# Optimization experiments

Hardware: AMD Instinct MI355X
Metric: run time of the kernel (lower is better)

The kernel has to match this reference:

```python
import jax, jax.numpy as jnp
import numpy as np

B, C, H, W = 4, 256, 64, 64
C8 = C // 8


def setup_inputs() -> dict:
    key = jax.random.key(0)
    ks = jax.random.split(key, 8)
    x = jax.random.normal(ks[0], (B, C, H, W), dtype=jnp.float32)
    # 1x1 conv weights act as per-pixel linear maps: [out_ch, in_ch]
    Wq = jax.random.normal(ks[1], (C8, C), dtype=jnp.float32) * 0.05
    bq = jax.random.normal(ks[2], (C8,), dtype=jnp.float32) * 0.01
    Wk = jax.random.normal(ks[3], (C8, C), dtype=jnp.float32) * 0.05
    bk = jax.random.normal(ks[4], (C8,), dtype=jnp.float32) * 0.01
    Wv = jax.random.normal(ks[5], (C, C), dtype=jnp.float32) * 0.05
    bv = jax.random.normal(ks[6], (C,), dtype=jnp.float32) * 0.01
    # torch inits gamma to 0 (identity); use nonzero so output exercises the attention path
    gamma = jnp.array(0.5, dtype=jnp.float32)
    return {"x": x, "Wq": Wq, "bq": bq, "Wk": Wk, "bk": bk, "Wv": Wv, "bv": bv, "gamma": gamma}


def reference(x, Wq, bq, Wk, bk, Wv, bv, gamma):
    b, c, h, w = x.shape
    n = h * w
    xf = x.reshape(b, c, n)                                   # [B,C,N]
    q = jnp.einsum('oc,bcn->bno', Wq, xf) + bq                # [B,N,C8] (proj_query permuted)
    k = jnp.einsum('oc,bcn->bon', Wk, xf) + bk[:, None]       # [B,C8,N]
    energy = jnp.einsum('bnc,bcm->bnm', q, k)                 # [B,N_q,N_k]
    # NOTE: torch Softmax(dim=1) -> normalize over the QUERY axis (axis=1)
    attention = jax.nn.softmax(energy, axis=1)
    v = jnp.einsum('oc,bcn->bon', Wv, xf) + bv[:, None]       # [B,C,N]
    out = jnp.einsum('bcn,bnm->bcm', v, attention).reshape(b, c, h, w)
    return gamma * out + x
```

## Files before the change

### kernel.cpp

```cpp
#include <hip/hip_runtime.h>
#include <hip/hip_bf16.h>

#define BN 4
#define CC 256
#define C8 32
#define NN 4096
#define PROJ_ROWS 320

typedef __attribute__((ext_vector_type(8))) short short8;
typedef __attribute__((ext_vector_type(4))) float f32x4;

__device__ __forceinline__ unsigned short f2bf(float f) {
    unsigned u = __builtin_bit_cast(unsigned, f);
    unsigned r = (u + 0x7fffu + ((u >> 16) & 1u)) >> 16;
    return (unsigned short)r;
}

__global__ __launch_bounds__(256) void proj_kernel(
    const float* __restrict__ x,
    const float* __restrict__ Wq, const float* __restrict__ bq,
    const float* __restrict__ Wk, const float* __restrict__ bk,
    const float* __restrict__ Wv, const float* __restrict__ bv,
    unsigned short* __restrict__ proj, unsigned short* __restrict__ qT)
{
    int bid = blockIdx.x;
    int b = bid >> 6, nt = bid & 63;
    int n0 = nt * 64;
    int tid = threadIdx.x;
    int w = tid >> 6, l = tid & 63, l15 = l & 15, lq = l >> 4;

    __shared__ alignas(16) unsigned short Xt[64][264];

    int c_l = tid >> 3;
    int nb  = (tid & 7) * 8;

#pragma unroll
    for (int kc = 0; kc < 8; kc++) {
        const float* xp = x + ((size_t)(b * CC + kc * 32 + c_l)) * NN + n0 + nb;
        float4 x0 = *(const float4*)xp;
        float4 x1 = *(const float4*)(xp + 4);
        float t[8] = {x0.x, x0.y, x0.z, x0.w, x1.x, x1.y, x1.z, x1.w};
#pragma unroll
        for (int e = 0; e < 8; e++) Xt[nb + e][kc * 32 + c_l] = f2bf(t[e]);
    }
    __syncthreads();

    f32x4 acc[5][4];
#pragma unroll
    for (int gi = 0; gi < 5; gi++)
#pragma unroll
        for (int mi = 0; mi < 4; mi++) acc[gi][mi] = (f32x4){0.f, 0.f, 0.f, 0.f};

    for (int kc = 0; kc < 8; kc++) {
        float4 wf[5][2];
#pragma unroll
        for (int gi = 0; gi < 5; gi++) {
            int og = (w * 5 + gi) * 16 + l15;
            const float* wrow = (og < 32) ? (Wq + (size_t)og * CC)
                              : (og < 64) ? (Wk + (size_t)(og - 32) * CC)
                                          : (Wv + (size_t)(og - 64) * CC);
            const float* wp = wrow + kc * 32 + lq * 8;
            wf[gi][0] = *(const float4*)wp;
            wf[gi][1] = *(const float4*)(wp + 4);
        }
#pragma unroll
        for (int gi = 0; gi < 5; gi++) {
            unsigned short a8[8] __attribute__((aligned(16)));
            float tw[8] = {wf[gi][0].x, wf[gi][0].y, wf[gi][0].z, wf[gi][0].w,
                           wf[gi][1].x, wf[gi][1].y, wf[gi][1].z, wf[gi][1].w};
#pragma unroll
            for (int e = 0; e < 8; e++) a8[e] = f2bf(tw[e]);
            short8 af = *(const short8*)a8;
#pragma unroll
            for (int mi = 0; mi < 4; mi++) {
                short8 bf = *(const short8*)&Xt[mi * 16 + l15][kc * 32 + lq * 8];
                acc[gi][mi] = __builtin_amdgcn_mfma_f32_16x16x32_bf16(af, bf, acc[gi][mi], 0, 0, 0);
            }
        }
    }

#pragma unroll
    for (int gi = 0; gi < 5; gi++) {
#pragma unroll
        for (int r = 0; r < 4; r++) {
            int og = (w * 5 + gi) * 16 + lq * 4 + r;
            float bias = (og < 32) ? bq[og] : (og < 64) ? bk[og - 32] : bv[og - 64];
#pragma unroll
            for (int mi = 0; mi < 4; mi++) {
                int n = n0 + mi * 16 + l15;
                unsigned short v16 = f2bf(acc[gi][mi][r] + bias);
                if (og < 32) {
                    qT[((size_t)b * NN + n) * C8 + og] = v16;
                } else {
                    proj[((size_t)b * PROJ_ROWS + og) * NN + n] = v16;
                }
            }
        }
    }
}

template<int NSPLIT, bool FINAL>
__global__ __launch_bounds__(256, 4) void attn_kernel(
    const unsigned short* __restrict__ proj,
    const unsigned short* __restrict__ qT,
    const float* __restrict__ x,
    const float* __restrict__ gamma_p,
    float* __restrict__ out,
    float* __restrict__ Opart,
    float* __restrict__ Lpart)
{
    constexpr int ITERS = 64 / NSPLIT;
    int bid = blockIdx.x;
    int h   = bid >> 8;
    int low = bid & 255;
    int xcd = low & 7;
    int b = xcd >> 1;
    int mtile = ((low >> 3) << 1) | (xcd & 1);
    int m0 = mtile * 64;
    int nbase = h * (ITERS * 64);

    int tid = threadIdx.x;
    int w = tid >> 6, l = tid & 63, l15 = l & 15, lq = l >> 4;

    __shared__ alignas(16) unsigned short ps[2][64][72];
    __shared__ float red[4][64];
    __shared__ float Ltot[64];

    const unsigned short* kbase = proj + ((size_t)b * PROJ_ROWS + C8) * NN;
    const unsigned short* vbase = proj + ((size_t)b * PROJ_ROWS + 64) * NN;
    const unsigned short* qbase = qT + (size_t)b * NN * C8;

    short8 kfrag[4];
#pragma unroll
    for (int mi = 0; mi < 4; mi++) {
        int col = m0 + mi * 16 + l15;
        unsigned short t8[8] __attribute__((aligned(16)));
#pragma unroll
        for (int j = 0; j < 8; j++)
            t8[j] = kbase[(size_t)(lq * 8 + j) * NN + col];
        kfrag[mi] = *(const short8*)t8;
    }

    f32x4 O[4][4];
#pragma unroll
    for (int ci = 0; ci < 4; ci++)
#pragma unroll
        for (int mi = 0; mi < 4; mi++) O[ci][mi] = (f32x4){0.f, 0.f, 0.f, 0.f};
    float runS[4] = {0.f, 0.f, 0.f, 0.f};

    {
        short8 qfrag = *(const short8*)(qbase + (size_t)(nbase + 16 * w + l15) * C8 + lq * 8);
#pragma unroll
        for (int mi = 0; mi < 4; mi++) {
            f32x4 S = __builtin_amdgcn_mfma_f32_16x16x32_bf16(
                qfrag, kfrag[mi], (f32x4){0.f, 0.f, 0.f, 0.f}, 0, 0, 0);
            float p0 = __expf(S[0]);
            float p1 = __expf(S[1]);
            float p2 = __expf(S[2]);
            float p3 = __expf(S[3]);
            runS[mi] += (p0 + p1) + (p2 + p3);
            unsigned pk0 = (unsigned)f2bf(p0) | ((unsigned)f2bf(p1) << 16);
            unsigned pk1 = (unsigned)f2bf(p2) | ((unsigned)f2bf(p3) << 16);
            *(uint2*)&ps[0][mi * 16 + l15][16 * w + lq * 4] = make_uint2(pk0, pk1);
        }
    }

    for (int it = 0; it < ITERS; it++) {
        int n0c = nbase + it * 64;
        __syncthreads();

        const unsigned short* psrc = &ps[it & 1][0][0];
#pragma unroll
        for (int kh = 0; kh < 2; kh++) {
            short8 av[4];
#pragma unroll
            for (int ci = 0; ci < 4; ci++)
                av[ci] = *(const short8*)(vbase
                         + (size_t)(64 * w + ci * 16 + l15) * NN + n0c + kh * 32 + lq * 8);
            short8 bfr[4];
#pragma unroll
            for (int mi = 0; mi < 4; mi++)
                bfr[mi] = *(const short8*)(psrc + (mi * 16 + l15) * 72 + kh * 32 + lq * 8);
#pragma unroll
            for (int ci = 0; ci < 4; ci++)
#pragma unroll
                for (int mi = 0; mi < 4; mi++)
                    O[ci][mi] = __builtin_amdgcn_mfma_f32_16x16x32_bf16(
                        av[ci], bfr[mi], O[ci][mi], 0, 0, 0);
        }

        if (it + 1 < ITERS) {
            short8 qfrag = *(const short8*)(qbase
                           + (size_t)(n0c + 64 + 16 * w + l15) * C8 + lq * 8);
            unsigned short* pdst = &ps[(it + 1) & 1][0][0];
#pragma unroll
            for (int mi = 0; mi < 4; mi++) {
                f32x4 S = __builtin_amdgcn_mfma_f32_16x16x32_bf16(
                    qfrag, kfrag[mi], (f32x4){0.f, 0.f, 0.f, 0.f}, 0, 0, 0);
                float p0 = __expf(S[0]);
                float p1 = __expf(S[1]);
                float p2 = __expf(S[2]);
                float p3 = __expf(S[3]);
                runS[mi] += (p0 + p1) + (p2 + p3);
                unsigned pk0 = (unsigned)f2bf(p0) | ((unsigned)f2bf(p1) << 16);
                unsigned pk1 = (unsigned)f2bf(p2) | ((unsigned)f2bf(p3) << 16);
                *(uint2*)(pdst + (mi * 16 + l15) * 72 + 16 * w + lq * 4) = make_uint2(pk0, pk1);
            }
        }
    }

#pragma unroll
    for (int mi = 0; mi < 4; mi++) {
        float s = runS[mi];
        s += __shfl_xor(s, 16);
        s += __shfl_xor(s, 32);
        red[w][mi * 16 + l15] = s;
    }
    __syncthreads();
    if (tid < 64) Ltot[tid] = red[0][tid] + red[1][tid] + red[2][tid] + red[3][tid];
    __syncthreads();

    if constexpr (FINAL) {
        float gamma = gamma_p[0];
        float iv[4];
#pragma unroll
        for (int mi = 0; mi < 4; mi++) iv[mi] = 1.0f / Ltot[mi * 16 + l15];
#pragma unroll
        for (int ci = 0; ci < 4; ci++) {
#pragma unroll
            for (int mi = 0; mi < 4; mi++) {
                int m = m0 + mi * 16 + l15;
#pragma unroll
                for (int r = 0; r < 4; r++) {
                    int c = 64 * w + ci * 16 + lq * 4 + r;
                    size_t idx = ((size_t)b * CC + c) * NN + m;
                    out[idx] = gamma * (O[ci][mi][r] * iv[mi]) + x[idx];
                }
            }
        }
    } else {
        size_t p = ((size_t)h * BN + b) * 64 + mtile;
        if (tid < 64) Lpart[p * 64 + tid] = Ltot[tid];
        float* Ob = Opart + p * (size_t)(CC * 64);
#pragma unroll
        for (int ci = 0; ci < 4; ci++) {
#pragma unroll
            for (int mi = 0; mi < 4; mi++) {
#pragma unroll
                for (int r = 0; r < 4; r++) {
                    int c = 64 * w + ci * 16 + lq * 4 + r;
                    Ob[c * 64 + mi * 16 + l15] = O[ci][mi][r];
                }
            }
        }
    }
}

template<int NSPLIT>
__global__ __launch_bounds__(256) void combine_kernel(
    const float* __restrict__ Opart, const float* __restrict__ Lpart,
    const float* __restrict__ x, const float* __restrict__ gamma_p,
    float* __restrict__ out)
{
    int bid = blockIdx.x;
    int cq = bid & 3;
    int mt = (bid >> 2) & 63;
    int b  = bid >> 8;
    int tid = threadIdx.x;
    int m4 = tid & 15, c16 = tid >> 4;
    float gamma = gamma_p[0];

    f32x4 Ls = (f32x4){0.f, 0.f, 0.f, 0.f};
#pragma unroll
    for (int h = 0; h < NSPLIT; h++) {
        size_t p = ((size_t)h * BN + b) * 64 + mt;
        Ls += *(const f32x4*)(Lpart + p * 64 + m4 * 4);
    }
    f32x4 inv;
#pragma unroll
    for (int j = 0; j < 4; j++) inv[j] = 1.0f / Ls[j];

#pragma unroll
    for (int cp = 0; cp < 4; cp++) {
        int c = cq * 64 + cp * 16 + c16;
        f32x4 acc = (f32x4){0.f, 0.f, 0.f, 0.f};
#pragma unroll
        for (int h = 0; h < NSPLIT; h++) {
            size_t p = ((size_t)h * BN + b) * 64 + mt;
            acc += *(const f32x4*)(Opart + p * (size_t)(CC * 64) + c * 64 + m4 * 4);
        }
        size_t idx = ((size_t)b * CC + c) * NN + mt * 64 + m4 * 4;
        f32x4 xv = *(const f32x4*)(x + idx);
        f32x4 o;
#pragma unroll
        for (int j = 0; j < 4; j++) o[j] = gamma * (acc[j] * inv[j]) + xv[j];
        *(f32x4*)(out + idx) = o;
    }
}

extern "C" void kernel_launch(void* const* d_in, const int* in_sizes, int n_in,
                              void* d_out, int out_size, void* d_ws, size_t ws_size,
                              hipStream_t stream) {
    const float* x     = (const float*)d_in[0];
    const float* Wq    = (const float*)d_in[1];
    const float* bq    = (const float*)d_in[2];
    const float* Wk    = (const float*)d_in[3];
    const float* bk    = (const float*)d_in[4];
    const float* Wv    = (const float*)d_in[5];
    const float* bv    = (const float*)d_in[6];
    const float* gamma = (const float*)d_in[7];
    float* out = (float*)d_out;
    (void)in_sizes; (void)n_in; (void)out_size;

    unsigned short* proj = (unsigned short*)d_ws;
    unsigned short* qT   = proj + (size_t)BN * PROJ_ROWS * NN;
    const size_t baseB = ((size_t)BN * PROJ_ROWS * NN + (size_t)BN * NN * C8) * 2;

    auto needB = [&](int ns) {
        size_t LpB = (size_t)ns * BN * 64 * 64 * 4;
        size_t OpB = (size_t)ns * BN * 64 * CC * 64 * 4;
        return baseB + LpB + OpB;
    };

    proj_kernel<<<256, 256, 0, stream>>>(x, Wq, bq, Wk, bk, Wv, bv, proj, qT);

    if (ws_size >= needB(4)) {
        float* Lpart = (float*)((char*)d_ws + baseB);
        float* Opart = Lpart + (size_t)4 * BN * 64 * 64;
        attn_kernel<4, false><<<1024, 256, 0, stream>>>(proj, qT, x, gamma, out, Opart, Lpart);
        combine_kernel<4><<<1024, 256, 0, stream>>>(Opart, Lpart, x, gamma, out);
    } else if (ws_size >= needB(2)) {
        float* Lpart = (float*)((char*)d_ws + baseB);
        float* Opart = Lpart + (size_t)2 * BN * 64 * 64;
        attn_kernel<2, false><<<512, 256, 0, stream>>>(proj, qT, x, gamma, out, Opart, Lpart);
        combine_kernel<2><<<1024, 256, 0, stream>>>(Opart, Lpart, x, gamma, out);
    } else {
        attn_kernel<1, true><<<256, 256, 0, stream>>>(proj, qT, x, gamma, out, nullptr, nullptr);
    }
}
```

Baseline: 181.7 us.

## Restructure attention into single-wave blocks with register-resident P and exp2 softmax

The attention kernel becomes one wavefront per block. Each block owns 128 channels and 64 key columns and walks the query axis 16 rows at a time. The P tile stays in registers and feeds a 16x16x16 MFMA directly, which removes the LDS round-trip and the per-iteration __syncthreads. V and Q fragments for the next step are prefetched into registers. The projection folds log2(e) into K so the kernel can use exp2f, and it now uses smaller 32-column tiles with twice as many blocks. The trade-offs are that every channel-half block recomputes the QK^T energies and the exponentials, and the kernel carries high register pressure from 32 accumulators plus the prefetch buffers.

```diff
diff --git a/kernel.cpp b/kernel.cpp
--- a/kernel.cpp
+++ b/kernel.cpp
@@ -6,14 +6,26 @@
 #define C8 32
 #define NN 4096
 #define PROJ_ROWS 320
+#define LOG2E 1.4426950408889634f
 
 typedef __attribute__((ext_vector_type(8))) short short8;
+typedef __attribute__((ext_vector_type(4))) short short4v;
 typedef __attribute__((ext_vector_type(4))) float f32x4;
+typedef __attribute__((ext_vector_type(2))) unsigned int uint2v;
 
 __device__ __forceinline__ unsigned short f2bf(float f) {
     unsigned u = __builtin_bit_cast(unsigned, f);
     unsigned r = (u + 0x7fffu + ((u >> 16) & 1u)) >> 16;
     return (unsigned short)r;
+}
+
+__device__ __forceinline__ f32x4 mfma16_bf16(short4v a, short4v b, f32x4 c) {
+#if __has_builtin(__builtin_amdgcn_mfma_f32_16x16x16bf16_1k)
+    return __builtin_amdgcn_mfma_f32_16x16x16bf16_1k(a, b, c, 0, 0, 0);
+#else
+    asm("v_mfma_f32_16x16x16_bf16 %0, %1, %2, %0" : "+v"(c) : "v"(a), "v"(b));
+    return c;
+#endif
 }
 
 __global__ __launch_bounds__(256) void proj_kernel(
@@ -24,32 +36,32 @@
     unsigned short* __restrict__ proj, unsigned short* __restrict__ qT)
 {
     int bid = blockIdx.x;
-    int b = bid >> 6, nt = bid & 63;
-    int n0 = nt * 64;
+    int b = bid >> 7, nt = bid & 127;
+    int n0 = nt * 32;
     int tid = threadIdx.x;
     int w = tid >> 6, l = tid & 63, l15 = l & 15, lq = l >> 4;
 
-    __shared__ alignas(16) unsigned short Xt[64][264];
+    __shared__ alignas(16) unsigned short Xt[32][264];
 
     int c_l = tid >> 3;
-    int nb  = (tid & 7) * 8;
+    int nb  = (tid & 7) * 4;
 
 #pragma unroll
     for (int kc = 0; kc < 8; kc++) {
         const float* xp = x + ((size_t)(b * CC + kc * 32 + c_l)) * NN + n0 + nb;
         float4 x0 = *(const float4*)xp;
-        float4 x1 = *(const float4*)(xp + 4);
-        float t[8] = {x0.x, x0.y, x0.z, x0.w, x1.x, x1.y, x1.z, x1.w};
-#pragma unroll
-        for (int e = 0; e < 8; e++) Xt[nb + e][kc * 32 + c_l] = f2bf(t[e]);
+        Xt[nb + 0][kc * 32 + c_l] = f2bf(x0.x);
+        Xt[nb + 1][kc * 32 + c_l] = f2bf(x0.y);
+        Xt[nb + 2][kc * 32 + c_l] = f2bf(x0.z);
+        Xt[nb + 3][kc * 32 + c_l] = f2bf(x0.w);
     }
     __syncthreads();
 
-    f32x4 acc[5][4];
+    f32x4 acc[5][2];
 #pragma unroll
     for (int gi = 0; gi < 5; gi++)
 #pragma unroll
-        for (int mi = 0; mi < 4; mi++) acc[gi][mi] = (f32x4){0.f, 0.f, 0.f, 0.f};
+        for (int mi = 0; mi < 2; mi++) acc[gi][mi] = (f32x4){0.f, 0.f, 0.f, 0.f};
 
     for (int kc = 0; kc < 8; kc++) {
         float4 wf[5][2];
@@ -72,7 +84,7 @@
             for (int e = 0; e < 8; e++) a8[e] = f2bf(tw[e]);
             short8 af = *(const short8*)a8;
 #pragma unroll
-            for (int mi = 0; mi < 4; mi++) {
+            for (int mi = 0; mi < 2; mi++) {
                 short8 bf = *(const short8*)&Xt[mi * 16 + l15][kc * 32 + lq * 8];
                 acc[gi][mi] = __builtin_amdgcn_mfma_f32_16x16x32_bf16(af, bf, acc[gi][mi], 0, 0, 0);
             }
@@ -85,10 +97,13 @@
         for (int r = 0; r < 4; r++) {
             int og = (w * 5 + gi) * 16 + lq * 4 + r;
             float bias = (og < 32) ? bq[og] : (og < 64) ? bk[og - 32] : bv[og - 64];
-#pragma unroll
-            for (int mi = 0; mi < 4; mi++) {
+            bool is_k = (og >= 32) && (og < 64);
+#pragma unroll
+            for (int mi = 0; mi < 2; mi++) {
                 int n = n0 + mi * 16 + l15;
-                unsigned short v16 = f2bf(acc[gi][mi][r] + bias);
+                float v = acc[gi][mi][r] + bias;
+                if (is_k) v *= LOG2E;
+                unsigned short v16 = f2bf(v);
                 if (og < 32) {
                     qT[((size_t)b * NN + n) * C8 + og] = v16;
                 } else {
@@ -100,7 +115,7 @@
 }
 
 template<int NSPLIT, bool FINAL>
-__global__ __launch_bounds__(256, 4) void attn_kernel(
+__global__ __launch_bounds__(64, 2) void attn_kernel(
     const unsigned short* __restrict__ proj,
     const unsigned short* __restrict__ qT,
     const float* __restrict__ x,
@@ -109,22 +124,20 @@
     float* __restrict__ Opart,
     float* __restrict__ Lpart)
 {
-    constexpr int ITERS = 64 / NSPLIT;
+    constexpr int ITERS = NN / NSPLIT / 16;
     int bid = blockIdx.x;
-    int h   = bid >> 8;
-    int low = bid & 255;
-    int xcd = low & 7;
-    int b = xcd >> 1;
-    int mtile = ((low >> 3) << 1) | (xcd & 1);
-    int m0 = mtile * 64;
-    int nbase = h * (ITERS * 64);
-
-    int tid = threadIdx.x;
-    int w = tid >> 6, l = tid & 63, l15 = l & 15, lq = l >> 4;
-
-    __shared__ alignas(16) unsigned short ps[2][64][72];
-    __shared__ float red[4][64];
-    __shared__ float Ltot[64];
+    int low = bid & 7;
+    int b = low >> 1, mhalf = low & 1;
+    int rest = bid >> 3;
+    int h  = rest % NSPLIT;
+    int ch = (rest / NSPLIT) & 1;
+    int mt = ((rest / (NSPLIT * 2)) << 1) | mhalf;
+    int m0 = mt * 64;
+    int c0 = ch * 128;
+    int nbase = h * (NN / NSPLIT);
+
+    int l = threadIdx.x;
+    int l15 = l & 15, lq = l >> 4;
 
     const unsigned short* kbase = proj + ((size_t)b * PROJ_ROWS + C8) * NN;
     const unsigned short* vbase = proj + ((size_t)b * PROJ_ROWS + 64) * NN;
@@ -141,71 +154,64 @@
         kfrag[mi] = *(const short8*)t8;
     }
 
-    f32x4 O[4][4];
-#pragma unroll
-    for (int ci = 0; ci < 4; ci++)
+    f32x4 O[8][4];
+#pragma unroll
+    for (int ci = 0; ci < 8; ci++)
 #pragma unroll
         for (int mi = 0; mi < 4; mi++) O[ci][mi] = (f32x4){0.f, 0.f, 0.f, 0.f};
     float runS[4] = {0.f, 0.f, 0.f, 0.f};
 
-    {
-        short8 qfrag = *(const short8*)(qbase + (size_t)(nbase + 16 * w + l15) * C8 + lq * 8);
+    uint2v av[8];
+#pragma unroll
+    for (int ci = 0; ci < 8; ci++)
+        av[ci] = *(const uint2v*)(vbase + (size_t)(c0 + ci * 16 + l15) * NN + nbase + lq * 4);
+    short8 qfrag = *(const short8*)(qbase + (size_t)(nbase + l15) * C8 + lq * 8);
+
+    for (int it = 0; it < ITERS; it++) {
+        int n0c = nbase + it * 16;
+
+        uint2v avn[8];
+        short8 qn;
+        if (it + 1 < ITERS) {
+            int nn = n0c + 16;
+#pragma unroll
+            for (int ci = 0; ci < 8; ci++)
+                avn[ci] = *(const uint2v*)(vbase + (size_t)(c0 + ci * 16 + l15) * NN + nn + lq * 4);
+            qn = *(const short8*)(qbase + (size_t)(nn + l15) * C8 + lq * 8);
+        }
+
+        f32x4 S[4];
+#pragma unroll
+        for (int mi = 0; mi < 4; mi++)
+            S[mi] = __builtin_amdgcn_mfma_f32_16x16x32_bf16(
+                qfrag, kfrag[mi], (f32x4){0.f, 0.f, 0.f, 0.f}, 0, 0, 0);
+
+        short4v pf[4];
 #pragma unroll
         for (int mi = 0; mi < 4; mi++) {
-            f32x4 S = __builtin_amdgcn_mfma_f32_16x16x32_bf16(
-                qfrag, kfrag[mi], (f32x4){0.f, 0.f, 0.f, 0.f}, 0, 0, 0);
-            float p0 = __expf(S[0]);
-            float p1 = __expf(S[1]);
-            float p2 = __expf(S[2]);
-            float p3 = __expf(S[3]);
+            float p0 = exp2f(S[mi][0]);
+            float p1 = exp2f(S[mi][1]);
+            float p2 = exp2f(S[mi][2]);
+            float p3 = exp2f(S[mi][3]);
             runS[mi] += (p0 + p1) + (p2 + p3);
-            unsigned pk0 = (unsigned)f2bf(p0) | ((unsigned)f2bf(p1) << 16);
-            unsigned pk1 = (unsigned)f2bf(p2) | ((unsigned)f2bf(p3) << 16);
-            *(uint2*)&ps[0][mi * 16 + l15][16 * w + lq * 4] = make_uint2(pk0, pk1);
-        }
-    }
-
-    for (int it = 0; it < ITERS; it++) {
-        int n0c = nbase + it * 64;
-        __syncthreads();
-
-        const unsigned short* psrc = &ps[it & 1][0][0];
-#pragma unroll
-        for (int kh = 0; kh < 2; kh++) {
-            short8 av[4];
-#pragma unroll
-            for (int ci = 0; ci < 4; ci++)
-                av[ci] = *(const short8*)(vbase
-                         + (size_t)(64 * w + ci * 16 + l15) * NN + n0c + kh * 32 + lq * 8);
-            short8 bfr[4];
+            uint2v u;
+            u.x = (unsigned)f2bf(p0) | ((unsigned)f2bf(p1) << 16);
+            u.y = (unsigned)f2bf(p2) | ((unsigned)f2bf(p3) << 16);
+            pf[mi] = __builtin_bit_cast(short4v, u);
+        }
+
+#pragma unroll
+        for (int ci = 0; ci < 8; ci++) {
+            short4v a = __builtin_bit_cast(short4v, av[ci]);
 #pragma unroll
             for (int mi = 0; mi < 4; mi++)
-                bfr[mi] = *(const short8*)(psrc + (mi * 16 + l15) * 72 + kh * 32 + lq * 8);
-#pragma unroll
-            for (int ci = 0; ci < 4; ci++)
-#pragma unroll
-                for (int mi = 0; mi < 4; mi++)
-                    O[ci][mi] = __builtin_amdgcn_mfma_f32_16x16x32_bf16(
-                        av[ci], bfr[mi], O[ci][mi], 0, 0, 0);
+                O[ci][mi] = mfma16_bf16(a, pf[mi], O[ci][mi]);
         }
 
         if (it + 1 < ITERS) {
-            short8 qfrag = *(const short8*)(qbase
-                           + (size_t)(n0c + 64 + 16 * w + l15) * C8 + lq * 8);
-            unsigned short* pdst = &ps[(it + 1) & 1][0][0];
-#pragma unroll
-            for (int mi = 0; mi < 4; mi++) {
-                f32x4 S = __builtin_amdgcn_mfma_f32_16x16x32_bf16(
-                    qfrag, kfrag[mi], (f32x4){0.f, 0.f, 0.f, 0.f}, 0, 0, 0);
-                float p0 = __expf(S[0]);
-                float p1 = __expf(S[1]);
-                float p2 = __expf(S[2]);
-                float p3 = __expf(S[3]);
-                runS[mi] += (p0 + p1) + (p2 + p3);
-                unsigned pk0 = (unsigned)f2bf(p0) | ((unsigned)f2bf(p1) << 16);
-                unsigned pk1 = (unsigned)f2bf(p2) | ((unsigned)f2bf(p3) << 16);
-                *(uint2*)(pdst + (mi * 16 + l15) * 72 + 16 * w + lq * 4) = make_uint2(pk0, pk1);
-            }
+#pragma unroll
+            for (int ci = 0; ci < 8; ci++) av[ci] = avn[ci];
+            qfrag = qn;
         }
     }
 
@@ -214,41 +220,42 @@
         float s = runS[mi];
         s += __shfl_xor(s, 16);
         s += __shfl_xor(s, 32);
-        red[w][mi * 16 + l15] = s;
-    }
-    __syncthreads();
-    if (tid < 64) Ltot[tid] = red[0][tid] + red[1][tid] + red[2][tid] + red[3][tid];
-    __syncthreads();
+        runS[mi] = s;
+    }
 
     if constexpr (FINAL) {
         float gamma = gamma_p[0];
         float iv[4];
 #pragma unroll
-        for (int mi = 0; mi < 4; mi++) iv[mi] = 1.0f / Ltot[mi * 16 + l15];
-#pragma unroll
-        for (int ci = 0; ci < 4; ci++) {
+        for (int mi = 0; mi < 4; mi++) iv[mi] = 1.0f / runS[mi];
+#pragma unroll
+        for (int ci = 0; ci < 8; ci++) {
 #pragma unroll
             for (int mi = 0; mi < 4; mi++) {
                 int m = m0 + mi * 16 + l15;
 #pragma unroll
                 for (int r = 0; r < 4; r++) {
-                    int c = 64 * w + ci * 16 + lq * 4 + r;
+                    int c = c0 + ci * 16 + lq * 4 + r;
                     size_t idx = ((size_t)b * CC + c) * NN + m;
                     out[idx] = gamma * (O[ci][mi][r] * iv[mi]) + x[idx];
                 }
             }
         }
     } else {
-        size_t p = ((size_t)h * BN + b) * 64 + mtile;
-        if (tid < 64) Lpart[p * 64 + tid] = Ltot[tid];
+        size_t p = ((size_t)h * BN + b) * 64 + mt;
+        if (ch == 0 && lq == 0) {
+#pragma unroll
+            for (int mi = 0; mi < 4; mi++)
+                Lpart[p * 64 + mi * 16 + l15] = runS[mi];
+        }
         float* Ob = Opart + p * (size_t)(CC * 64);
 #pragma unroll
-        for (int ci = 0; ci < 4; ci++) {
+        for (int ci = 0; ci < 8; ci++) {
 #pragma unroll
             for (int mi = 0; mi < 4; mi++) {
 #pragma unroll
                 for (int r = 0; r < 4; r++) {
-                    int c = 64 * w + ci * 16 + lq * 4 + r;
+                    int c = c0 + ci * 16 + lq * 4 + r;
                     Ob[c * 64 + mi * 16 + l15] = O[ci][mi][r];
                 }
             }
@@ -322,19 +329,19 @@
         return baseB + LpB + OpB;
     };
 
-    proj_kernel<<<256, 256, 0, stream>>>(x, Wq, bq, Wk, bk, Wv, bv, proj, qT);
+    proj_kernel<<<512, 256, 0, stream>>>(x, Wq, bq, Wk, bk, Wv, bv, proj, qT);
 
     if (ws_size >= needB(4)) {
         float* Lpart = (float*)((char*)d_ws + baseB);
         float* Opart = Lpart + (size_t)4 * BN * 64 * 64;
-        attn_kernel<4, false><<<1024, 256, 0, stream>>>(proj, qT, x, gamma, out, Opart, Lpart);
+        attn_kernel<4, false><<<2048, 64, 0, stream>>>(proj, qT, x, gamma, out, Opart, Lpart);
         combine_kernel<4><<<1024, 256, 0, stream>>>(Opart, Lpart, x, gamma, out);
     } else if (ws_size >= needB(2)) {
         float* Lpart = (float*)((char*)d_ws + baseB);
         float* Opart = Lpart + (size_t)2 * BN * 64 * 64;
-        attn_kernel<2, false><<<512, 256, 0, stream>>>(proj, qT, x, gamma, out, Opart, Lpart);
+        attn_kernel<2, false><<<1024, 64, 0, stream>>>(proj, qT, x, gamma, out, Opart, Lpart);
         combine_kernel<2><<<1024, 256, 0, stream>>>(Opart, Lpart, x, gamma, out);
     } else {
-        attn_kernel<1, true><<<256, 256, 0, stream>>>(proj, qT, x, gamma, out, nullptr, nullptr);
-    }
-}
+        attn_kernel<1, true><<<512, 64, 0, stream>>>(proj, qT, x, gamma, out, nullptr, nullptr);
+    }
+}
```

New measurement: 245.1 us. 34.9% more time.
